# Optimization experiments

Measured on AMD Instinct MI355X. Metric: run time of the kernel, lower is better.

Reference implementation:

```python
import jax, jax.numpy as jnp
import numpy as np

B, N, K, A = 2, 4096, 20, 12
DIMS = [32, 64, 128, 256, 512]
POOL_RATE, POOL_K = 4, 4


def knn_index(v, k):
    # v: (b, n, 3) -> (b, n, k) nearest neighbors, self excluded
    d2 = jnp.sum(v * v, axis=-1)
    dist = d2[:, :, None] + d2[:, None, :] - 2.0 * jnp.einsum('bnd,bmd->bnm', v, v)
    _, idx = jax.lax.top_k(-dist, k + 1)
    return idx[:, :, 1:]


def gather_pos(v, idx):
    return jax.vmap(lambda vv, ii: vv[ii])(v, idx)  # (b, n, k, 3)


def gather_fea(fm, idx):
    return jax.vmap(lambda f, ii: f[:, ii, :])(fm, idx)  # (b, c, n, k, a)


def nbr_dirs(v, idx):
    d = gather_pos(v, idx) - v[:, :, None, :]
    return d / (jnp.linalg.norm(d, axis=-1, keepdims=True) + 1e-8)


def conv_surface(idx, v, K0):
    # K0: (C0, A, 3) learned direction kernels; output (b, C0, n, A)
    d = nbr_dirs(v, idx)  # (b,n,k,3)
    theta = jax.nn.relu(jnp.einsum('bnkd,cad->bnkca', d, K0))
    return jnp.transpose(jnp.max(theta, axis=2), (0, 2, 1, 3))


def equi_conv(idx, v, fm, dirs, Wc, bc, Ws):
    # fm: (b, cin, n, a) -> (b, cout, n, a)
    d = nbr_dirs(v, idx)
    theta = jax.nn.relu(jnp.einsum('bnkd,ad->bnka', d, dirs))  # (b,n,k,a)
    fn = gather_fea(fm, idx)  # (b,cin,n,k,a)
    fs = jnp.einsum('bcnka,co->bonka', fn, Ws) * theta[:, None]
    fs = jnp.max(fs, axis=3)  # max over neighbors -> (b,cout,n,a)
    fc = jnp.einsum('bcna,co->bona', fm, Wc) + bc[None, :, None, None]
    return fc + fs


def batchnorm(x, g, b):
    m = jnp.mean(x, axis=(0, 2, 3), keepdims=True)
    var = jnp.var(x, axis=(0, 2, 3), keepdims=True)
    return (x - m) * jax.lax.rsqrt(var + 1e-5) * g[None, :, None, None] + b[None, :, None, None]


def pool(v, fm):
    idx = knn_index(v, POOL_K)
    fn = jnp.max(gather_fea(fm, idx), axis=3)
    fm_p = jnp.maximum(fm, fn)
    sel = jnp.arange(0, v.shape[1], POOL_RATE)  # strided subsample
    return v[:, sel], fm_p[:, :, sel]


def fea_of(fm):
    return jnp.transpose(jnp.max(fm, axis=-1), (0, 2, 1))  # (b,n,c)


def setup_inputs() -> dict:
    key = jax.random.key(0)
    ks = iter(jax.random.split(key, 32))
    p = {'vertices': jax.random.normal(next(ks), (B, N, 3), jnp.float32)}
    p['K0'] = jax.random.normal(next(ks), (DIMS[0], A, 3), jnp.float32) * 0.1
    for i, (ci, co) in enumerate(zip(DIMS[:4], DIMS[1:]), start=1):
        s = 1.0 / np.sqrt(ci).astype(np.float32)
        p[f'dirs{i}'] = jax.random.normal(next(ks), (A, 3), jnp.float32) * 0.1
        p[f'Wc{i}'] = jax.random.normal(next(ks), (ci, co), jnp.float32) * s
        p[f'bc{i}'] = jnp.zeros((co,), jnp.float32)
        p[f'Ws{i}'] = jax.random.normal(next(ks), (ci, co), jnp.float32) * s
    for i, c in enumerate([DIMS[1], DIMS[2], DIMS[3]], start=1):
        p[f'g{i}'] = jnp.ones((c,), jnp.float32)
        p[f'b{i}'] = jnp.zeros((c,), jnp.float32)
    return p


def reference(vertices, K0, dirs1, Wc1, bc1, Ws1, dirs2, Wc2, bc2, Ws2,
              dirs3, Wc3, bc3, Ws3, dirs4, Wc4, bc4, Ws4,
              g1, b1, g2, b2, g3, b3):
    idx = knn_index(vertices, K)
    fm0 = jax.nn.relu(conv_surface(idx, vertices, K0))
    fm1 = jax.nn.relu(batchnorm(equi_conv(idx, vertices, fm0, dirs1, Wc1, bc1, Ws1), g1, b1))
    v1, fmp1 = pool(vertices, fm1)
    idx1 = knn_index(v1, min(K, v1.shape[1] // 8))
    fm2 = jax.nn.relu(batchnorm(equi_conv(idx1, v1, fmp1, dirs2, Wc2, bc2, Ws2), g2, b2))
    fm3 = jax.nn.relu(batchnorm(equi_conv(idx1, v1, fm2, dirs3, Wc3, bc3, Ws3), g3, b3))
    v2, fmp2 = pool(v1, fm3)
    idx2 = knn_index(v2, min(K, v2.shape[1] // 8))
    fm4 = equi_conv(idx2, v2, fmp2, dirs4, Wc4, bc4, Ws4)
    return fea_of(fm0), fea_of(fm1), fea_of(fm2), fea_of(fm3), fea_of(fm4)
```

## Files before the change

kernel.cpp:

```cpp
#include <hip/hip_runtime.h>
#include <hip/hip_bf16.h>
#include <math.h>

typedef unsigned short u16;
typedef unsigned long long u64;
#define DEV static __device__ __forceinline__

constexpr int Bz = 2, N0 = 4096, N1 = 1024, N2 = 256, KNN = 20, NA = 12;
constexpr int C0 = 32, C1 = 64, C2 = 128, C3 = 256, C4 = 512;
constexpr int BNG = 32;

constexpr size_t OFF_V0F   = 0;
constexpr size_t OFF_V1F   = 32768;
constexpr size_t OFF_V2F   = 40960;
constexpr size_t OFF_K0F   = 43008;
constexpr size_t OFF_DIRS  = 44160;
constexpr size_t OFF_WC    = 44304;
constexpr size_t OFF_WS    = 218384;
constexpr size_t OFF_BC    = 392464;
constexpr size_t OFF_BN    = 393424;
constexpr size_t OFF_FLAG  = 394832;
constexpr size_t OFF_IDX0  = 394848;
constexpr size_t OFF_IDX1  = 558688;
constexpr size_t OFF_IDX2  = 599648;
constexpr size_t OFF_PART  = 609888;
constexpr size_t PART_SZ   = 28672;
constexpr size_t OFF_HALF  = OFF_PART + PART_SZ;

constexpr size_t HA = 0;
constexpr size_t HB = 3145728;
constexpr size_t HG = 9437184;
constexpr size_t HP = HG + 3145728;
constexpr size_t WTO = 15728640;

constexpr size_t OUT0 = 0;
constexpr size_t OUT1 = OUT0 + (size_t)Bz*N0*C0;
constexpr size_t OUT2 = OUT1 + (size_t)Bz*N0*C1;
constexpr size_t OUT3 = OUT2 + (size_t)Bz*N1*C2;
constexpr size_t OUT4 = OUT3 + (size_t)Bz*N1*C3;

DEV float b2f(u16 v) { return __uint_as_float(((unsigned int)v) << 16); }
DEV u16 f2b(float f) {
  unsigned int u = __float_as_uint(f);
  unsigned int lsb = (u >> 16) & 1u;
  return (u16)((u + 0x7fffu + lsb) >> 16);
}
DEV unsigned packb(float a, float b) {
  return (unsigned)f2b(a) | ((unsigned)f2b(b) << 16);
}

DEV u64 shflx64(u64 v, int m) {
  int lo = __shfl_xor((int)(unsigned)v, m, 64);
  int hi = __shfl_xor((int)(unsigned)(v >> 32), m, 64);
  return ((u64)(unsigned)hi << 32) | (unsigned)lo;
}
DEV int mbcnt64(u64 m) {
  return __builtin_amdgcn_mbcnt_hi((unsigned)(m >> 32),
         __builtin_amdgcn_mbcnt_lo((unsigned)m, 0));
}

DEV void st12(float* dst, const float* v) {
  float4 a{v[0],v[1],v[2],v[3]}, b{v[4],v[5],v[6],v[7]}, c{v[8],v[9],v[10],v[11]};
  ((float4*)dst)[0] = a; ((float4*)dst)[1] = b; ((float4*)dst)[2] = c;
}
DEV void st12(u16* dst, const float* v) {
  uint2 a{packb(v[0],v[1]), packb(v[2],v[3])};
  uint2 b{packb(v[4],v[5]), packb(v[6],v[7])};
  uint2 c{packb(v[8],v[9]), packb(v[10],v[11])};
  ((uint2*)dst)[0] = a; ((uint2*)dst)[1] = b; ((uint2*)dst)[2] = c;
}

struct InPtrs { const void* p[24]; };

__global__ void eq_convert_all(InPtrs in, float* ws) {
  __shared__ int sflag;
  {
    const u16* v = (const u16*)in.p[0];
    if (threadIdx.x < 64) {
      int bad = 0;
      #pragma unroll
      for (int j = 0; j < 4; ++j) {
        unsigned u = v[threadIdx.x*4 + j];
        int ex = (u >> 7) & 0xFF;
        bad += (((u & 0x7FFFu) != 0u) && (ex < 64 || ex > 191)) ? 1 : 0;
      }
      int tot = bad;
      #pragma unroll
      for (int s = 32; s > 0; s >>= 1) tot += __shfl_xor(tot, s, 64);
      if (threadIdx.x == 0) sflag = (tot >= 8) ? 1 : 0;
    }
    __syncthreads();
  }
  int f32mode = sflag;
  int t = blockIdx.x * blockDim.x + threadIdx.x;
  if (t < Bz*N0) {
    float x, y, z;
    if (f32mode) { const float* v = (const float*)in.p[0]; x=v[t*3]; y=v[t*3+1]; z=v[t*3+2]; }
    else { const u16* v = (const u16*)in.p[0]; x=b2f(v[t*3]); y=b2f(v[t*3+1]); z=b2f(v[t*3+2]); }
    float4 o; o.x=x; o.y=y; o.z=z; o.w=(x*x + y*y) + z*z;
    ((float4*)(ws + OFF_V0F))[t] = o;
    int b = t / N0, i = t % N0;
    if ((i & 3) == 0)  ((float4*)(ws + OFF_V1F))[b*N1 + (i >> 2)] = o;
    if ((i & 15) == 0) ((float4*)(ws + OFF_V2F))[b*N2 + (i >> 4)] = o;
    return;
  }
  int r = t - Bz*N0;
  if (r >= 351312) {
    int z = r - 351312;
    if (z < (int)PART_SZ) ws[OFF_PART + z] = 0.f;
    return;
  }
  const int cnt[23] = {1152, 36,2048,64,2048, 36,8192,128,8192,
                       36,32768,256,32768, 36,131072,512,131072,
                       64,64,128,128,256,256};
  const size_t off[23] = {OFF_K0F,
    OFF_DIRS+0,   OFF_WC+0,     OFF_BC+0,   OFF_WS+0,
    OFF_DIRS+36,  OFF_WC+2048,  OFF_BC+64,  OFF_WS+2048,
    OFF_DIRS+72,  OFF_WC+10240, OFF_BC+192, OFF_WS+10240,
    OFF_DIRS+108, OFF_WC+43008, OFF_BC+448, OFF_WS+43008,
    OFF_BN+0, OFF_BN+64, OFF_BN+128, OFF_BN+256, OFF_BN+384, OFF_BN+640};
  for (int i = 0; i < 23; ++i) {
    if (r < cnt[i]) {
      float val = f32mode ? ((const float*)in.p[i+1])[r] : b2f(((const u16*)in.p[i+1])[r]);
      ws[off[i] + r] = val;
      return;
    }
    r -= cnt[i];
  }
}

__global__ void eq_wprep(const float* __restrict__ ws,
    u16* __restrict__ ch, u16* __restrict__ cl,
    u16* __restrict__ sh, u16* __restrict__ sl) {
  int e = blockIdx.x*256 + threadIdx.x;
  if (e >= 174080) return;
  const int co[4] = {64,128,256,512};
  const int ci[4] = {32,64,128,256};
  const int off[4] = {0,2048,10240,43008};
  int li = 0, loc = e;
  if (e >= 43008) { li = 3; loc = e - 43008; }
  else if (e >= 10240) { li = 2; loc = e - 10240; }
  else if (e >= 2048) { li = 1; loc = e - 2048; }
  int c = loc / co[li], o = loc % co[li];
  size_t dst = (size_t)off[li] + (size_t)o*ci[li] + c;
  float wc = ws[OFF_WC + e];
  u16 h = f2b(wc); u16 l = f2b(wc - b2f(h));
  ch[dst] = h; cl[dst] = l;
  float wv = ws[OFF_WS + e];
  h = f2b(wv); l = f2b(wv - b2f(h));
  sh[dst] = h; sl[dst] = l;
}

DEV unsigned cand_ud(const float4 vq, const float4 vc) {
  float dt = fmaf(vq.x, vc.x, fmaf(vq.y, vc.y, vq.z*vc.z));
  float d  = fmaf(-2.0f, dt, vq.w + vc.w);
  unsigned u = __float_as_uint(d);
  return u ^ ((unsigned)(((int)u) >> 31) | 0x80000000u);
}

#define INSA(u,c) do { bool lt1=(u)<dA1, lt2=(u)<dA2, lt3=(u)<dA3, lt4=(u)<dA4; \
  dA4=lt3?dA3:(lt4?(u):dA4); iA4=lt3?iA3:(lt4?(c):iA4); \
  dA3=lt2?dA2:(lt3?(u):dA3); iA3=lt2?iA2:(lt3?(c):iA3); \
  dA2=lt1?dA1:(lt2?(u):dA2); iA2=lt1?iA1:(lt2?(c):iA2); \
  dA1=lt1?(u):dA1;           iA1=lt1?(c):iA1; } while(0)
#define INSB(u,c) do { bool lt1=(u)<dB1, lt2=(u)<dB2, lt3=(u)<dB3, lt4=(u)<dB4; \
  dB4=lt3?dB3:(lt4?(u):dB4); iB4=lt3?iB3:(lt4?(c):iB4); \
  dB3=lt2?dB2:(lt3?(u):dB3); iB3=lt2?iB2:(lt3?(c):iB3); \
  dB2=lt1?dB1:(lt2?(u):dB2); iB2=lt1?iB1:(lt2?(c):iB2); \
  dB1=lt1?(u):dB1;           iB1=lt1?(c):iB1; } while(0)

#define CMP1(uu,cc) do { bool sel=(uu)<=p; u64 m=__ballot(sel); \
  int pos = base2 + mbcnt64(m); \
  if (sel && pos < 128) selw[pos] = ((u64)(uu) << 32) | (unsigned)(cc); \
  base2 += __popcll(m); } while(0)

template<int NPTS>
DEV void knn_body(int blk, const float4* __restrict__ vf, int* __restrict__ idx_out,
                  char* smem) {
  constexpr int CPL = NPTS/64;
  constexpr int HC  = CPL/2;
  int wave = threadIdx.x >> 6, lane = threadIdx.x & 63;
  u64* selw = (u64*)smem + wave*128;
  int* extrw = (int*)(smem + 4*128*8) + wave*24;
  int qid = blk*4 + wave;
  int b = qid / NPTS, q = qid % NPTS;
  const float4* vb = vf + (size_t)b*NPTS;
  float4 vq = vb[q];

  unsigned dA1=~0u,dA2=~0u,dA3=~0u,dA4=~0u; int iA1=0,iA2=0,iA3=0,iA4=0;
  unsigned dB1=~0u,dB2=~0u,dB3=~0u,dB4=~0u; int iB1=0,iB2=0,iB3=0,iB4=0;

  if (CPL >= 8) {
    for (int jb = 0; jb < CPL; jb += 8) {
      int base = jb*64 + lane;
      float4 c0 = vb[base];
      float4 c1 = vb[base + 64];
      float4 c2 = vb[base + 128];
      float4 c3 = vb[base + 192];
      float4 c4 = vb[base + 256];
      float4 c5 = vb[base + 320];
      float4 c6 = vb[base + 384];
      float4 c7 = vb[base + 448];
      unsigned u0 = cand_ud(vq, c0);
      unsigned u1 = cand_ud(vq, c1);
      unsigned u2 = cand_ud(vq, c2);
      unsigned u3 = cand_ud(vq, c3);
      unsigned u4 = cand_ud(vq, c4);
      unsigned u5 = cand_ud(vq, c5);
      unsigned u6 = cand_ud(vq, c6);
      unsigned u7 = cand_ud(vq, c7);
      INSA(u0, base);       INSB(u1, base + 64);
      INSA(u2, base + 128); INSB(u3, base + 192);
      INSA(u4, base + 256); INSB(u5, base + 320);
      INSA(u6, base + 384); INSB(u7, base + 448);
    }
  } else {
    int base = lane;
    float4 c0 = vb[base];
    float4 c1 = vb[base + 64];
    float4 c2 = vb[base + 128];
    float4 c3 = vb[base + 192];
    unsigned u0 = cand_ud(vq, c0);
    unsigned u1 = cand_ud(vq, c1);
    unsigned u2 = cand_ud(vq, c2);
    unsigned u3 = cand_ud(vq, c3);
    INSA(u0, base);       INSB(u1, base + 64);
    INSA(u2, base + 128); INSB(u3, base + 192);
  }

  unsigned p = 0;
  for (int bit = 31; bit >= 0; --bit) {
    unsigned T = p | (1u << bit);
    int cnt = __popcll(__ballot(dA1 < T)) + __popcll(__ballot(dA2 < T))
            + __popcll(__ballot(dA3 < T)) + __popcll(__ballot(dA4 < T))
            + __popcll(__ballot(dB1 < T)) + __popcll(__ballot(dB2 < T))
            + __popcll(__ballot(dB3 < T)) + __popcll(__ballot(dB4 < T));
    if (cnt < KNN+1) p = T;
  }
  size_t obase = (size_t)qid*KNN;
  bool need_fb = (HC > 4) &&
                 ((__ballot(dA4 <= p) | __ballot(dB4 <= p)) != 0ULL);

  if (!need_fb) {
    bool pA1=dA1<=p, pA2=dA2<=p, pA3=dA3<=p, pA4=dA4<=p;
    bool pB1=dB1<=p, pB2=dB2<=p, pB3=dB3<=p, pB4=dB4<=p;
    u64 m1=__ballot(pA1), m2=__ballot(pA2), m3=__ballot(pA3), m4=__ballot(pA4);
    u64 m5=__ballot(pB1), m6=__ballot(pB2), m7=__ballot(pB3), m8=__ballot(pB4);
    int c1=__popcll(m1), c2=__popcll(m2), c3=__popcll(m3), c4=__popcll(m4);
    int c5=__popcll(m5), c6=__popcll(m6), c7=__popcll(m7), c8=__popcll(m8);
    int S = ((c1+c2)+(c3+c4)) + ((c5+c6)+(c7+c8));
    if (S > 127) need_fb = true;
    else {
      int o1=c1, o2=o1+c2, o3=o2+c3, o4=o3+c4, o5=o4+c5, o6=o5+c6, o7=o6+c7;
      if (pA1) selw[mbcnt64(m1)]      = ((u64)dA1 << 32) | (unsigned)iA1;
      if (pA2) selw[o1 + mbcnt64(m2)] = ((u64)dA2 << 32) | (unsigned)iA2;
      if (pA3) selw[o2 + mbcnt64(m3)] = ((u64)dA3 << 32) | (unsigned)iA3;
      if (pA4) selw[o3 + mbcnt64(m4)] = ((u64)dA4 << 32) | (unsigned)iA4;
      if (pB1) selw[o4 + mbcnt64(m5)] = ((u64)dB1 << 32) | (unsigned)iB1;
      if (pB2) selw[o5 + mbcnt64(m6)] = ((u64)dB2 << 32) | (unsigned)iB2;
      if (pB3) selw[o6 + mbcnt64(m7)] = ((u64)dB3 << 32) | (unsigned)iB3;
      if (pB4) selw[o7 + mbcnt64(m8)] = ((u64)dB4 << 32) | (unsigned)iB4;
      for (int sl = lane; sl < S; sl += 64) {
        u64 mykey = selw[sl];
        int rank = 0;
        for (int j2 = 0; j2 < S; ++j2) rank += (selw[j2] < mykey) ? 1 : 0;
        if (rank >= 1 && rank <= KNN)
          idx_out[obase + rank - 1] = (int)(unsigned)(mykey & 0xFFFFFFFFu);
      }
    }
  }
  if (need_fb && CPL >= 8) {
    int base2 = 0;
    for (int jb = 0; jb < CPL; jb += 8) {
      int bidx = jb*64 + lane;
      float4 c0 = vb[bidx];
      float4 c1 = vb[bidx + 64];
      float4 c2 = vb[bidx + 128];
      float4 c3 = vb[bidx + 192];
      float4 c4 = vb[bidx + 256];
      float4 c5 = vb[bidx + 320];
      float4 c6 = vb[bidx + 384];
      float4 c7 = vb[bidx + 448];
      unsigned u0 = cand_ud(vq, c0);
      unsigned u1 = cand_ud(vq, c1);
      unsigned u2 = cand_ud(vq, c2);
      unsigned u3 = cand_ud(vq, c3);
      unsigned u4 = cand_ud(vq, c4);
      unsigned u5 = cand_ud(vq, c5);
      unsigned u6 = cand_ud(vq, c6);
      unsigned u7 = cand_ud(vq, c7);
      CMP1(u0, bidx);       CMP1(u1, bidx + 64);
      CMP1(u2, bidx + 128); CMP1(u3, bidx + 192);
      CMP1(u4, bidx + 256); CMP1(u5, bidx + 320);
      CMP1(u6, bidx + 384); CMP1(u7, bidx + 448);
    }
    if (base2 <= 127) {
      int S = base2;
      for (int sl = lane; sl < S; sl += 64) {
        u64 mykey = selw[sl];
        int rank = 0;
        for (int j2 = 0; j2 < S; ++j2) rank += (selw[j2] < mykey) ? 1 : 0;
        if (rank >= 1 && rank <= KNN)
          idx_out[obase + rank - 1] = (int)(unsigned)(mykey & 0xFFFFFFFFu);
      }
    } else {
      const u64 KINF = ~0ULL;
      u64 K1=KINF, K2=KINF, K3=KINF, K4=KINF;
      for (int j = 0; j < CPL; ++j) {
        int c = j*64 + lane;
        u64 k = ((u64)cand_ud(vq, vb[c]) << 32) | (unsigned)c;
        bool lt1 = k < K1, lt2 = k < K2, lt3 = k < K3, lt4 = k < K4;
        K4 = lt3 ? K3 : (lt4 ? k : K4);
        K3 = lt2 ? K2 : (lt3 ? k : K3);
        K2 = lt1 ? K1 : (lt2 ? k : K2);
        K1 = lt1 ? k  : K1;
      }
      for (int r = 0; r < KNN+1; ++r) {
        u64 g = K1;
        #pragma unroll
        for (int s = 32; s; s >>= 1) { u64 o = shflx64(g, s); g = (o < g) ? o : g; }
        int gidx = (int)(unsigned)(g & 0xFFFFFFFFu);
        if (lane == 0) {
          extrw[r] = gidx;
          if (r > 0) idx_out[obase + r - 1] = gidx;
        }
        if (r < KNN && lane == (gidx & 63)) {
          K1 = K2; K2 = K3; K3 = K4; K4 = KINF;
          if (K1 == KINF) {
            for (int j = 0; j < CPL; ++j) {
              int c = j*64 + lane;
              u64 k = ((u64)cand_ud(vq, vb[c]) << 32) | (unsigned)c;
              bool ex = false;
              for (int e = 0; e <= r; ++e) ex |= (extrw[e] == c);
              if (!ex) {
                bool lt1 = k < K1, lt2 = k < K2, lt3 = k < K3, lt4 = k < K4;
                K4 = lt3 ? K3 : (lt4 ? k : K4);
                K3 = lt2 ? K2 : (lt3 ? k : K3);
                K2 = lt1 ? K1 : (lt2 ? k : K2);
                K1 = lt1 ? k  : K1;
              }
            }
          }
        }
      }
    }
  }
}

__global__ __launch_bounds__(256) void eq_knn_all(
    const float4* __restrict__ v0, int* __restrict__ i0,
    const float4* __restrict__ v1, int* __restrict__ i1,
    const float4* __restrict__ v2, int* __restrict__ i2) {
  __shared__ __align__(16) char smem[4*128*8 + 4*24*4];
  int blk = blockIdx.x;
  constexpr int NB0 = Bz*N0/4, NB1 = Bz*N1/4;
  if (blk < NB0)            knn_body<N0>(blk, v0, i0, smem);
  else if (blk < NB0+NB1)   knn_body<N1>(blk - NB0, v1, i1, smem);
  else                      knn_body<N2>(blk - NB0 - NB1, v2, i2, smem);
}

__global__ __launch_bounds__(128) void eq_conv_surface(
    const float4* __restrict__ v0f, const int* __restrict__ idx0,
    const float* __restrict__ K0f, u16* __restrict__ fm0, float* __restrict__ out0) {
  int bq = blockIdx.x;
  int b = bq >> 12;
  __shared__ float dk[KNN][3];
  __shared__ float row[C0*NA];
  int tid = threadIdx.x;
  if (tid < KNN) {
    int m = idx0[(size_t)bq*KNN + tid];
    float4 vq = v0f[bq];
    float4 vm = v0f[(size_t)b*N0 + m];
    float dx = vm.x - vq.x, dy = vm.y - vq.y, dz = vm.z - vq.z;
    float nrm = sqrtf((dx*dx + dy*dy) + dz*dz) + 1e-8f;
    dk[tid][0] = dx/nrm; dk[tid][1] = dy/nrm; dk[tid][2] = dz/nrm;
  }
  __syncthreads();
  for (int t4 = tid; t4 < C0*NA/4; t4 += 128) {
    const float* kd = K0f + (size_t)t4*12;
    float4 k0 = *(const float4*)(kd);
    float4 k1 = *(const float4*)(kd + 4);
    float4 k2 = *(const float4*)(kd + 8);
    float m0=0.f, m1=0.f, m2=0.f, m3=0.f;
    #pragma unroll
    for (int k = 0; k < KNN; ++k) {
      float dx = dk[k][0], dy = dk[k][1], dz = dk[k][2];
      m0 = fmaxf(m0, (dx*k0.x + dy*k0.y) + dz*k0.z);
      m1 = fmaxf(m1, (dx*k0.w + dy*k1.x) + dz*k1.y);
      m2 = fmaxf(m2, (dx*k1.z + dy*k1.w) + dz*k2.x);
      m3 = fmaxf(m3, (dx*k2.y + dy*k2.z) + dz*k2.w);
    }
    uint2 r; r.x = packb(m0, m1); r.y = packb(m2, m3);
    ((uint2*)fm0)[(size_t)bq*(C0*NA/4) + t4] = r;
    row[4*t4+0] = m0; row[4*t4+1] = m1; row[4*t4+2] = m2; row[4*t4+3] = m3;
  }
  __syncthreads();
  if (tid < C0) {
    float m = row[tid*NA];
    #pragma unroll
    for (int a = 1; a < NA; ++a) m = fmaxf(m, row[tid*NA + a]);
    out0[(size_t)bq*C0 + tid] = m;
  }
}

typedef __attribute__((ext_vector_type(8))) short bf16x8;
typedef __attribute__((ext_vector_type(4))) float f32x4;

DEV void store1(float* p, float v) { *p = v; }
DEV void store1(u16* p, float v) { *p = f2b(v); }

template<int CI, int CO, int PT, typename TO>
__global__ __launch_bounds__(256) void eq_linear_mfma(
    const u16* __restrict__ in,
    const u16* __restrict__ wc_hi, const u16* __restrict__ wc_lo,
    const u16* __restrict__ ws_hi, const u16* __restrict__ ws_lo,
    const float* __restrict__ bias, TO* __restrict__ fc, u16* __restrict__ g) {
  constexpr int MR = 12*PT;
  constexpr int TM = MR/16;
  constexpr int TN = CO/16;
  constexpr int KF = CI/32;
  constexpr int RS = CI + 8;
  __shared__ u16 As[MR*RS];
  int tid = threadIdx.x;
  int mat = blockIdx.x & 1;
  int pt0 = (blockIdx.x >> 1) * PT;
  constexpr int EU = PT*CI*12/2;
  const unsigned* inw = (const unsigned*)(in + (size_t)pt0*CI*12);
  for (int t = tid; t < EU; t += 256) {
    unsigned v = inw[t];
    int e = 2*t;
    int pt = e / (CI*12), r = e % (CI*12);
    int c = r / 12, a = r % 12;
    As[(a*PT + pt)*RS + c] = (u16)v;
    As[((a+1)*PT + pt)*RS + c] = (u16)(v >> 16);
  }
  __syncthreads();
  int wave = tid >> 6, lane = tid & 63;
  int lr = lane & 15;
  int lk = lane >> 4;
  const u16* Whi = mat ? ws_hi : wc_hi;
  const u16* Wlo = mat ? ws_lo : wc_lo;
  for (int tp = wave; tp < TM*TN; tp += 4) {
    int mt = tp % TM, nt = tp / TM;
    int n0 = nt*16;
    f32x4 acc = {0.f, 0.f, 0.f, 0.f};
    #pragma unroll
    for (int kf = 0; kf < KF; ++kf) {
      bf16x8 af = *(const bf16x8*)&As[(mt*16 + lr)*RS + kf*32 + lk*8];
      bf16x8 bh = *(const bf16x8*)&Whi[(size_t)(n0 + lr)*CI + kf*32 + lk*8];
      bf16x8 bl = *(const bf16x8*)&Wlo[(size_t)(n0 + lr)*CI + kf*32 + lk*8];
      acc = __builtin_amdgcn_mfma_f32_16x16x32_bf16(af, bh, acc, 0, 0, 0);
      acc = __builtin_amdgcn_mfma_f32_16x16x32_bf16(af, bl, acc, 0, 0, 0);
    }
    int n = n0 + lr;
    float bv = (mat == 0) ? bias[n] : 0.f;
    #pragma unroll
    for (int j = 0; j < 4; ++j) {
      int m = mt*16 + lk*4 + j;
      int a = m / PT, pt = m % PT;
      float v = acc[j] + bv;
      size_t oaddr = ((size_t)(pt0 + pt)*CO + n)*NA + a;
      if (mat == 0) store1(fc + oaddr, v);
      else          store1(g + oaddr, v);
    }
  }
}

__global__ __launch_bounds__(256) void eq_fsmax(
    const u16* __restrict__ g, const float4* __restrict__ vf,
    const float* __restrict__ dirs, const int* __restrict__ idx,
    u16* __restrict__ out, float* __restrict__ part, int npts, int co) {
  int bq = blockIdx.x;
  int b = bq / npts;
  __shared__ float th[KNN*NA];
  __shared__ float dk[KNN][3];
  __shared__ int nb[KNN];
  __shared__ float sstat[2][C3];
  int tid = threadIdx.x;
  if (tid < KNN) {
    int m = idx[(size_t)bq*KNN + tid];
    nb[tid] = m;
    float4 vq = vf[bq];
    float4 vm = vf[(size_t)b*npts + m];
    float dx = vm.x - vq.x, dy = vm.y - vq.y, dz = vm.z - vq.z;
    float nrm = sqrtf((dx*dx + dy*dy) + dz*dz) + 1e-8f;
    dk[tid][0] = dx/nrm; dk[tid][1] = dy/nrm; dk[tid][2] = dz/nrm;
  }
  sstat[0][tid] = 0.f; sstat[1][tid] = 0.f;
  __syncthreads();
  if (tid < KNN*NA) {
    int k = tid / NA, a = tid % NA;
    float s = (dk[k][0]*dirs[a*3] + dk[k][1]*dirs[a*3+1]) + dk[k][2]*dirs[a*3+2];
    th[tid] = fmaxf(s, 0.f);
  }
  __syncthreads();
  int quarter = co*NA/4;
  uint2* dst = (uint2*)(out + (size_t)bq*co*NA);
  const uint2* gb = (const uint2*)(g + (size_t)b*npts*co*NA);
  for (int t4 = tid; t4 < quarter; t4 += 256) {
    int a = (4*t4) % NA;
    const float* tha = th + a;
    float m0=-3.0e38f, m1=-3.0e38f, m2=-3.0e38f, m3=-3.0e38f;
    #pragma unroll 5
    for (int k = 0; k < KNN; ++k) {
      uint2 pv = gb[(size_t)nb[k]*quarter + t4];
      float4 tv = *(const float4*)(tha + k*NA);
      m0 = fmaxf(m0, tv.x*b2f((u16)(pv.x)));
      m1 = fmaxf(m1, tv.y*b2f((u16)(pv.x >> 16)));
      m2 = fmaxf(m2, tv.z*b2f((u16)(pv.y)));
      m3 = fmaxf(m3, tv.w*b2f((u16)(pv.y >> 16)));
    }
    uint2 d = dst[t4];
    float v0 = b2f((u16)d.x) + m0;
    float v1 = b2f((u16)(d.x >> 16)) + m1;
    float v2 = b2f((u16)d.y) + m2;
    float v3 = b2f((u16)(d.y >> 16)) + m3;
    uint2 r; r.x = packb(v0, v1); r.y = packb(v2, v3);
    dst[t4] = r;
    int ch = t4 / 3;
    atomicAdd(&sstat[0][ch], (v0 + v1) + (v2 + v3));
    atomicAdd(&sstat[1][ch], (v0*v0 + v1*v1) + (v2*v2 + v3*v3));
  }
  __syncthreads();
  if (tid < co) {
    float* pg = part + (size_t)(bq & (BNG-1))*2*co;
    atomicAdd(&pg[tid], sstat[0][tid]);
    atomicAdd(&pg[co + tid], sstat[1][tid]);
  }
}

template<int SPL>
__global__ __launch_bounds__(256) void eq_fsmax_fea(
    const u16* __restrict__ g, const float* __restrict__ fcin,
    const float4* __restrict__ vf, const float* __restrict__ dirs,
    const int* __restrict__ idx, float* __restrict__ outfea,
    int npts, int co) {
  constexpr int CHUNK = C4 / SPL;
  int part = blockIdx.x % SPL;
  int bq = blockIdx.x / SPL;
  int b = bq / npts;
  __shared__ float th[KNN*NA];
  __shared__ float dk[KNN][3];
  __shared__ int nb[KNN];
  __shared__ float row[CHUNK*NA];
  int tid = threadIdx.x;
  if (tid < KNN) {
    int m = idx[(size_t)bq*KNN + tid];
    nb[tid] = m;
    float4 vq = vf[bq];
    float4 vm = vf[(size_t)b*npts + m];
    float dx = vm.x - vq.x, dy = vm.y - vq.y, dz = vm.z - vq.z;
    float nrm = sqrtf((dx*dx + dy*dy) + dz*dz) + 1e-8f;
    dk[tid][0] = dx/nrm; dk[tid][1] = dy/nrm; dk[tid][2] = dz/nrm;
  }
  __syncthreads();
  if (tid < KNN*NA) {
    int k = tid / NA, a = tid % NA;
    float s = (dk[k][0]*dirs[a*3] + dk[k][1]*dirs[a*3+1]) + dk[k][2]*dirs[a*3+2];
    th[tid] = fmaxf(s, 0.f);
  }
  __syncthreads();
  int o0 = part * CHUNK;
  const float4* fcr = (const float4*)(fcin + ((size_t)bq*co + o0)*NA);
  const uint2* gb = (const uint2*)(g + (size_t)b*npts*co*NA + (size_t)o0*NA);
  int gquarter = co*NA/4;
  for (int t4 = tid; t4 < CHUNK*NA/4; t4 += 256) {
    int a = (4*t4) % NA;
    const float* tha = th + a;
    float m0=-3.0e38f, m1=-3.0e38f, m2=-3.0e38f, m3=-3.0e38f;
    #pragma unroll 5
    for (int k = 0; k < KNN; ++k) {
      uint2 pv = gb[(size_t)nb[k]*gquarter + t4];
      float4 tv = *(const float4*)(tha + k*NA);
      m0 = fmaxf(m0, tv.x*b2f((u16)(pv.x)));
      m1 = fmaxf(m1, tv.y*b2f((u16)(pv.x >> 16)));
      m2 = fmaxf(m2, tv.z*b2f((u16)(pv.y)));
      m3 = fmaxf(m3, tv.w*b2f((u16)(pv.y >> 16)));
    }
    float4 fc4 = fcr[t4];
    row[4*t4+0] = fc4.x + m0;
    row[4*t4+1] = fc4.y + m1;
    row[4*t4+2] = fc4.z + m2;
    row[4*t4+3] = fc4.w + m3;
  }
  __syncthreads();
  for (int o = tid; o < CHUNK; o += 256) {
    float m = row[o*NA];
    #pragma unroll
    for (int a = 1; a < NA; ++a) m = fmaxf(m, row[o*NA + a]);
    outfea[(size_t)bq*co + o0 + o] = m;
  }
}

__global__ __launch_bounds__(256) void eq_bnrelu_fea(
    u16* __restrict__ fm, const float* __restrict__ part,
    const float* __restrict__ gamma, const float* __restrict__ beta,
    float* __restrict__ outfea, int npts, int co) {
  int bq = blockIdx.x;
  int tid = threadIdx.x;
  __shared__ float sc[C3], sh[C3];
  __shared__ float row[C3*NA];
  for (int o = tid; o < co; o += 256) {
    float s = 0.f, s2 = 0.f;
    for (int g = 0; g < BNG; ++g) {
      s  += part[(size_t)g*2*co + o];
      s2 += part[(size_t)g*2*co + co + o];
    }
    float cnt = (float)(Bz*npts*NA);
    float mean = s / cnt;
    float var = fmaxf(s2 / cnt - mean*mean, 0.f);
    float inv = 1.0f / sqrtf(var + 1e-5f);
    sc[o] = gamma[o] * inv;
    sh[o] = beta[o] - mean * gamma[o] * inv;
  }
  __syncthreads();
  uint2* p = (uint2*)(fm + (size_t)bq*co*NA);
  int quarter = co*NA/4;
  for (int t4 = tid; t4 < quarter; t4 += 256) {
    int o = (4*t4) / NA;
    float s = sc[o], h = sh[o];
    uint2 pv = p[t4];
    float v0 = fmaxf(b2f((u16)pv.x)*s + h, 0.f);
    float v1 = fmaxf(b2f((u16)(pv.x >> 16))*s + h, 0.f);
    float v2 = fmaxf(b2f((u16)pv.y)*s + h, 0.f);
    float v3 = fmaxf(b2f((u16)(pv.y >> 16))*s + h, 0.f);
    uint2 r; r.x = packb(v0, v1); r.y = packb(v2, v3);
    p[t4] = r;
    row[4*t4+0] = v0; row[4*t4+1] = v1; row[4*t4+2] = v2; row[4*t4+3] = v3;
  }
  __syncthreads();
  for (int o = tid; o < co; o += 256) {
    float m = row[o*NA];
    #pragma unroll
    for (int a = 1; a < NA; ++a) m = fmaxf(m, row[o*NA + a]);
    outfea[(size_t)bq*co + o] = m;
  }
}

__global__ __launch_bounds__(256) void eq_bnfea_pool(
    const u16* __restrict__ fm, const float* __restrict__ part,
    const float* __restrict__ gamma, const float* __restrict__ beta,
    const int* __restrict__ idx, float* __restrict__ outfea,
    u16* __restrict__ fmp, int npts, int co) {
  int bq = blockIdx.x;
  int b = bq / npts, q = bq % npts;
  int tid = threadIdx.x;
  __shared__ float sc[C3], sh[C3];
  __shared__ float row[C3*NA];
  __shared__ int nb[4];
  for (int o = tid; o < co; o += 256) {
    float s = 0.f, s2 = 0.f;
    for (int g = 0; g < BNG; ++g) {
      s  += part[(size_t)g*2*co + o];
      s2 += part[(size_t)g*2*co + co + o];
    }
    float cnt = (float)(Bz*npts*NA);
    float mean = s / cnt;
    float var = fmaxf(s2 / cnt - mean*mean, 0.f);
    float inv = 1.0f / sqrtf(var + 1e-5f);
    sc[o] = gamma[o] * inv;
    sh[o] = beta[o] - mean * gamma[o] * inv;
  }
  bool do_pool = ((q & 3) == 0);
  if (do_pool && tid < 4) nb[tid] = idx[(size_t)bq*KNN + tid];
  __syncthreads();
  int quarter = co*NA/4;
  const uint2* own = (const uint2*)(fm + (size_t)bq*co*NA);
  const uint2* base = (const uint2*)(fm + (size_t)b*npts*co*NA);
  uint2* dst = (uint2*)(fmp + ((size_t)b*(npts/4) + (q >> 2))*co*NA);
  for (int t4 = tid; t4 < quarter; t4 += 256) {
    int o = (4*t4) / NA;
    float s = sc[o], h = sh[o];
    uint2 pv = own[t4];
    float v0 = fmaxf(b2f((u16)pv.x)*s + h, 0.f);
    float v1 = fmaxf(b2f((u16)(pv.x >> 16))*s + h, 0.f);
    float v2 = fmaxf(b2f((u16)pv.y)*s + h, 0.f);
    float v3 = fmaxf(b2f((u16)(pv.y >> 16))*s + h, 0.f);
    row[4*t4+0] = v0; row[4*t4+1] = v1; row[4*t4+2] = v2; row[4*t4+3] = v3;
    if (do_pool) {
      float m0=v0, m1=v1, m2=v2, m3=v3;
      #pragma unroll
      for (int kk = 0; kk < 4; ++kk) {
        uint2 w = base[(size_t)nb[kk]*quarter + t4];
        m0 = fmaxf(m0, fmaxf(b2f((u16)w.x)*s + h, 0.f));
        m1 = fmaxf(m1, fmaxf(b2f((u16)(w.x >> 16))*s + h, 0.f));
        m2 = fmaxf(m2, fmaxf(b2f((u16)w.y)*s + h, 0.f));
        m3 = fmaxf(m3, fmaxf(b2f((u16)(w.y >> 16))*s + h, 0.f));
      }
      uint2 r; r.x = packb(m0, m1); r.y = packb(m2, m3);
      dst[t4] = r;
    }
  }
  __syncthreads();
  for (int o = tid; o < co; o += 256) {
    float m = row[o*NA];
    #pragma unroll
    for (int a = 1; a < NA; ++a) m = fmaxf(m, row[o*NA + a]);
    outfea[(size_t)bq*co + o] = m;
  }
}

extern "C" void kernel_launch(void* const* d_in, const int* in_sizes, int n_in,
                              void* d_out, int out_size, void* d_ws, size_t ws_size,
                              hipStream_t stream) {
  float* ws = (float*)d_ws;
  float* out = (float*)d_out;
  u16* arena = (u16*)(ws + OFF_HALF);

  InPtrs ip;
  for (int i = 0; i < 24; ++i) ip.p[i] = d_in[i];

  float4* v0f = (float4*)(ws + OFF_V0F);
  float4* v1f = (float4*)(ws + OFF_V1F);
  float4* v2f = (float4*)(ws + OFF_V2F);
  int* idx0 = (int*)(ws + OFF_IDX0);
  int* idx1 = (int*)(ws + OFF_IDX1);
  int* idx2 = (int*)(ws + OFF_IDX2);
  u16* bufA = arena + HA;
  u16* bufB = arena + HB;
  float* fc4f = (float*)(arena + HB);
  u16* bufG = arena + HG;
  u16* bufP = arena + HP;
  u16* wch = arena + WTO;
  u16* wcl = wch + 174080;
  u16* wsh = wcl + 174080;
  u16* wsl = wsh + 174080;
  float* partA = ws + OFF_PART;
  float* partB = ws + OFF_PART + 4096;
  float* partC = ws + OFF_PART + 12288;
  const float* DIRS = ws + OFF_DIRS;

  {
    int total = Bz*N0 + 351312 + (int)PART_SZ;
    eq_convert_all<<<(total + 255)/256, 256, 0, stream>>>(ip, ws);
  }
  eq_wprep<<<(174080 + 255)/256, 256, 0, stream>>>(ws, wch, wcl, wsh, wsl);

  eq_knn_all<<<Bz*N0/4 + Bz*N1/4 + Bz*N2/4, 256, 0, stream>>>(v0f, idx0, v1f, idx1, v2f, idx2);
  eq_conv_surface<<<Bz*N0, 128, 0, stream>>>(v0f, idx0, ws + OFF_K0F, bufA, out + OUT0);

  eq_linear_mfma<C0, C1, 8, u16><<<(Bz*N0/8)*2, 256, 0, stream>>>(
      bufA, wch + 0, wcl + 0, wsh + 0, wsl + 0, ws + OFF_BC + 0, bufB, bufG);
  eq_fsmax<<<Bz*N0, 256, 0, stream>>>(bufG, v0f, DIRS + 0, idx0, bufB, partA, N0, C1);
  eq_bnfea_pool<<<Bz*N0, 256, 0, stream>>>(bufB, partA, ws + OFF_BN + 0, ws + OFF_BN + 64,
                                           idx0, out + OUT1, bufP, N0, C1);

  eq_linear_mfma<C1, C2, 8, u16><<<(Bz*N1/8)*2, 256, 0, stream>>>(
      bufP, wch + 2048, wcl + 2048, wsh + 2048, wsl + 2048, ws + OFF_BC + 64, bufA, bufG);
  eq_fsmax<<<Bz*N1, 256, 0, stream>>>(bufG, v1f, DIRS + 36, idx1, bufA, partB, N1, C2);
  eq_bnrelu_fea<<<Bz*N1, 256, 0, stream>>>(bufA, partB, ws + OFF_BN + 128, ws + OFF_BN + 256,
                                           out + OUT2, N1, C2);

  eq_linear_mfma<C2, C3, 8, u16><<<(Bz*N1/8)*2, 256, 0, stream>>>(
      bufA, wch + 10240, wcl + 10240, wsh + 10240, wsl + 10240, ws + OFF_BC + 192, bufB, bufG);
  eq_fsmax<<<Bz*N1, 256, 0, stream>>>(bufG, v1f, DIRS + 72, idx1, bufB, partC, N1, C3);
  eq_bnfea_pool<<<Bz*N1, 256, 0, stream>>>(bufB, partC, ws + OFF_BN + 384, ws + OFF_BN + 640,
                                           idx1, out + OUT3, bufP, N1, C3);

  eq_linear_mfma<C3, C4, 4, float><<<(Bz*N2/4)*2, 256, 0, stream>>>(
      bufP, wch + 43008, wcl + 43008, wsh + 43008, wsl + 43008, ws + OFF_BC + 448, fc4f, bufG);
  eq_fsmax_fea<4><<<Bz*N2*4, 256, 0, stream>>>(bufG, fc4f, v2f, DIRS + 108, idx2, out + OUT4, N2, C4);
}
```

Measured before the change: 474.4 us.

## Split MFMA linear over output-channel chunks and keep weights in registers

```diff
diff --git a/kernel.cpp b/kernel.cpp
--- a/kernel.cpp
+++ b/kernel.cpp
@@ -409,7 +409,7 @@
 DEV void store1(float* p, float v) { *p = v; }
 DEV void store1(u16* p, float v) { *p = f2b(v); }
 
-template<int CI, int CO, int PT, typename TO>
+template<int CI, int CO, int PT, int SPLITN, typename TO>
 __global__ __launch_bounds__(256) void eq_linear_mfma(
     const u16* __restrict__ in,
     const u16* __restrict__ wc_hi, const u16* __restrict__ wc_lo,
@@ -418,12 +418,15 @@
   constexpr int MR = 12*PT;
   constexpr int TM = MR/16;
   constexpr int TN = CO/16;
+  constexpr int NTC = TN/SPLITN;
   constexpr int KF = CI/32;
   constexpr int RS = CI + 8;
   __shared__ u16 As[MR*RS];
   int tid = threadIdx.x;
   int mat = blockIdx.x & 1;
-  int pt0 = (blockIdx.x >> 1) * PT;
+  int rest = blockIdx.x >> 1;
+  int sp = rest % SPLITN;
+  int pt0 = (rest / SPLITN) * PT;
   constexpr int EU = PT*CI*12/2;
   const unsigned* inw = (const unsigned*)(in + (size_t)pt0*CI*12);
   for (int t = tid; t < EU; t += 256) {
@@ -440,28 +443,34 @@
   int lk = lane >> 4;
   const u16* Whi = mat ? ws_hi : wc_hi;
   const u16* Wlo = mat ? ws_lo : wc_lo;
-  for (int tp = wave; tp < TM*TN; tp += 4) {
-    int mt = tp % TM, nt = tp / TM;
-    int n0 = nt*16;
-    f32x4 acc = {0.f, 0.f, 0.f, 0.f};
+  for (int ntl = wave; ntl < NTC; ntl += 4) {
+    int nt = sp*NTC + ntl;
+    int n = nt*16 + lr;
+    bf16x8 bh[KF], bl[KF];
     #pragma unroll
     for (int kf = 0; kf < KF; ++kf) {
-      bf16x8 af = *(const bf16x8*)&As[(mt*16 + lr)*RS + kf*32 + lk*8];
-      bf16x8 bh = *(const bf16x8*)&Whi[(size_t)(n0 + lr)*CI + kf*32 + lk*8];
-      bf16x8 bl = *(const bf16x8*)&Wlo[(size_t)(n0 + lr)*CI + kf*32 + lk*8];
-      acc = __builtin_amdgcn_mfma_f32_16x16x32_bf16(af, bh, acc, 0, 0, 0);
-      acc = __builtin_amdgcn_mfma_f32_16x16x32_bf16(af, bl, acc, 0, 0, 0);
-    }
-    int n = n0 + lr;
+      bh[kf] = *(const bf16x8*)&Whi[(size_t)n*CI + kf*32 + lk*8];
+      bl[kf] = *(const bf16x8*)&Wlo[(size_t)n*CI + kf*32 + lk*8];
+    }
     float bv = (mat == 0) ? bias[n] : 0.f;
     #pragma unroll
-    for (int j = 0; j < 4; ++j) {
-      int m = mt*16 + lk*4 + j;
-      int a = m / PT, pt = m % PT;
-      float v = acc[j] + bv;
-      size_t oaddr = ((size_t)(pt0 + pt)*CO + n)*NA + a;
-      if (mat == 0) store1(fc + oaddr, v);
-      else          store1(g + oaddr, v);
+    for (int mt = 0; mt < TM; ++mt) {
+      f32x4 acc = {0.f, 0.f, 0.f, 0.f};
+      #pragma unroll
+      for (int kf = 0; kf < KF; ++kf) {
+        bf16x8 af = *(const bf16x8*)&As[(mt*16 + lr)*RS + kf*32 + lk*8];
+        acc = __builtin_amdgcn_mfma_f32_16x16x32_bf16(af, bh[kf], acc, 0, 0, 0);
+        acc = __builtin_amdgcn_mfma_f32_16x16x32_bf16(af, bl[kf], acc, 0, 0, 0);
+      }
+      #pragma unroll
+      for (int j = 0; j < 4; ++j) {
+        int m = mt*16 + lk*4 + j;
+        int a = m / PT, pt = m % PT;
+        float v = acc[j] + bv;
+        size_t oaddr = ((size_t)(pt0 + pt)*CO + n)*NA + a;
+        if (mat == 0) store1(fc + oaddr, v);
+        else          store1(g + oaddr, v);
+      }
     }
   }
 }
@@ -739,25 +748,25 @@
   eq_knn_all<<<Bz*N0/4 + Bz*N1/4 + Bz*N2/4, 256, 0, stream>>>(v0f, idx0, v1f, idx1, v2f, idx2);
   eq_conv_surface<<<Bz*N0, 128, 0, stream>>>(v0f, idx0, ws + OFF_K0F, bufA, out + OUT0);
 
-  eq_linear_mfma<C0, C1, 8, u16><<<(Bz*N0/8)*2, 256, 0, stream>>>(
+  eq_linear_mfma<C0, C1, 8, 1, u16><<<(Bz*N0/8)*2*1, 256, 0, stream>>>(
       bufA, wch + 0, wcl + 0, wsh + 0, wsl + 0, ws + OFF_BC + 0, bufB, bufG);
   eq_fsmax<<<Bz*N0, 256, 0, stream>>>(bufG, v0f, DIRS + 0, idx0, bufB, partA, N0, C1);
   eq_bnfea_pool<<<Bz*N0, 256, 0, stream>>>(bufB, partA, ws + OFF_BN + 0, ws + OFF_BN + 64,
                                            idx0, out + OUT1, bufP, N0, C1);
 
-  eq_linear_mfma<C1, C2, 8, u16><<<(Bz*N1/8)*2, 256, 0, stream>>>(
+  eq_linear_mfma<C1, C2, 8, 2, u16><<<(Bz*N1/8)*2*2, 256, 0, stream>>>(
       bufP, wch + 2048, wcl + 2048, wsh + 2048, wsl + 2048, ws + OFF_BC + 64, bufA, bufG);
   eq_fsmax<<<Bz*N1, 256, 0, stream>>>(bufG, v1f, DIRS + 36, idx1, bufA, partB, N1, C2);
   eq_bnrelu_fea<<<Bz*N1, 256, 0, stream>>>(bufA, partB, ws + OFF_BN + 128, ws + OFF_BN + 256,
                                            out + OUT2, N1, C2);
 
-  eq_linear_mfma<C2, C3, 8, u16><<<(Bz*N1/8)*2, 256, 0, stream>>>(
+  eq_linear_mfma<C2, C3, 8, 4, u16><<<(Bz*N1/8)*2*4, 256, 0, stream>>>(
       bufA, wch + 10240, wcl + 10240, wsh + 10240, wsl + 10240, ws + OFF_BC + 192, bufB, bufG);
   eq_fsmax<<<Bz*N1, 256, 0, stream>>>(bufG, v1f, DIRS + 72, idx1, bufB, partC, N1, C3);
   eq_bnfea_pool<<<Bz*N1, 256, 0, stream>>>(bufB, partC, ws + OFF_BN + 384, ws + OFF_BN + 640,
                                            idx1, out + OUT3, bufP, N1, C3);
 
-  eq_linear_mfma<C3, C4, 4, float><<<(Bz*N2/4)*2, 256, 0, stream>>>(
+  eq_linear_mfma<C3, C4, 4, 8, float><<<(Bz*N2/4)*2*8, 256, 0, stream>>>(
       bufP, wch + 43008, wcl + 43008, wsh + 43008, wsl + 43008, ws + OFF_BC + 448, fc4f, bufG);
   eq_fsmax_fea<4><<<Bz*N2*4, 256, 0, stream>>>(bufG, fc4f, v2f, DIRS + 108, idx2, out + OUT4, N2, C4);
 }
```

Result: faster. 412.6 us (-13.0%).
